# Kernel optimization log

Measured on AMD Instinct MI355X. Metric: run time of the kernel, lower is better.

Reference implementation:

```python
import jax, jax.numpy as jnp
import numpy as np

N_EMBED = 1024
HEAD_SIZE = 128

def setup_inputs() -> dict:
    key = jax.random.key(0)
    kx, kq, kk, kv = jax.random.split(key, 4)
    B, T = 8, 2048
    x = jax.random.normal(kx, (B, T, N_EMBED), dtype=jnp.float32)
    s = 1.0 / np.sqrt(N_EMBED)
    Wq = jax.random.normal(kq, (N_EMBED, HEAD_SIZE), dtype=jnp.float32) * s
    Wk = jax.random.normal(kk, (N_EMBED, HEAD_SIZE), dtype=jnp.float32) * s
    Wv = jax.random.normal(kv, (N_EMBED, HEAD_SIZE), dtype=jnp.float32) * s
    return {"x": x, "Wq": Wq, "Wk": Wk, "Wv": Wv}

def reference(x, Wq, Wk, Wv):
    # x: [B, T, E]; single-head causal attention (nanoGPT-style Head)
    B, T, E = x.shape
    q = jnp.einsum('bte,eh->bth', x, Wq)  # [B,T,H]
    k = jnp.einsum('bte,eh->bth', x, Wk)
    v = jnp.einsum('bte,eh->bth', x, Wv)
    scale = 1.0 / jnp.sqrt(jnp.asarray(q.shape[-1], dtype=x.dtype))
    wei = jnp.einsum('bqh,bkh->bqk', q, k) * scale  # [B,T,T]
    causal = jnp.tril(jnp.ones((T, T), dtype=bool))
    wei = jnp.where(causal[None, :, :], wei, jnp.asarray(-jnp.inf, dtype=wei.dtype))
    attn = jax.nn.softmax(wei, axis=-1)
    out = jnp.einsum('bqk,bkh->bqh', attn, v)  # [B,T,H]
    return out
```

## Files before the change

### kernel.cpp

```cpp
#include <hip/hip_runtime.h>
#include <hip/hip_bf16.h>

typedef __bf16 bf16_t;
typedef bf16_t bf16x8 __attribute__((ext_vector_type(8)));
typedef bf16_t bf16x4 __attribute__((ext_vector_type(4)));
typedef float f32x4 __attribute__((ext_vector_type(4)));

#define MFMA16(a, b, c) __builtin_amdgcn_mfma_f32_16x16x32_bf16((a), (b), (c), 0, 0, 0)

#define TT 2048
#define EE 1024
#define HH 128
#define UPB 576


__global__ __launch_bounds__(256) void prep_w_kernel(
    const float* __restrict__ Wq, const float* __restrict__ Wk,
    const float* __restrict__ Wv, bf16_t* __restrict__ Wf)
{
    int idx = blockIdx.x * 256 + threadIdx.x;
    int e  = idx & 7;
    int c  = (idx >> 3) & 15;
    int g  = (idx >> 7) & 3;
    int kt = (idx >> 9) & 31;
    int ct = idx >> 14;
    int w  = ct >> 3;
    const float* W = (w == 0) ? Wq : (w == 1) ? Wk : Wv;
    int k = kt * 32 + g * 8 + e;
    int n = (ct & 7) * 16 + c;
    Wf[idx] = (bf16_t)W[k * HH + n];
}

__global__ __launch_bounds__(256) void qkv_kernel(
    const float* __restrict__ x, const bf16_t* __restrict__ Wf,
    bf16_t* __restrict__ Qf, bf16_t* __restrict__ Kf, bf16_t* __restrict__ Vf)
{
    __shared__ __attribute__((aligned(16))) bf16_t As[2][64][72];
    const int bx = blockIdx.x;
    const int row0  = (bx & 255) * 64;
    const int nhalf = bx >> 8;
    const int tid  = threadIdx.x;
    const int lane = tid & 63;
    const int wn   = tid >> 6;
    const int g = lane >> 4, c = lane & 15;

    const int srow = tid >> 2;
    const int scg  = tid & 3;
    const float* xp = x + (size_t)(row0 + srow) * EE + scg * 16;

    const bf16_t* wfb = Wf + ((size_t)(nhalf * 12 + wn * 3) * 32) * 512 + lane * 8;

    f32x4 acc[4][3];
    for (int i = 0; i < 4; ++i)
        for (int j = 0; j < 3; ++j) acc[i][j] = (f32x4)0.0f;

    f32x4 xa[3][4];
    bf16x8 w[2][6];

#define BAR() do {                                                            \
    asm volatile("s_waitcnt lgkmcnt(0)" ::: "memory");                        \
    __builtin_amdgcn_s_barrier();                                             \
    __builtin_amdgcn_sched_barrier(0);                                        \
} while (0)
#define XLOAD(S, T)                                                           \
    for (int q = 0; q < 4; ++q)                                               \
        xa[S][q] = *(const f32x4*)(xp + (size_t)(T) * 64 + q * 4);
#define WLOAD(S, T)                                                           \
    for (int kk = 0; kk < 2; ++kk)                                            \
        for (int j = 0; j < 3; ++j)                                           \
            w[S][kk * 3 + j] = *(const bf16x8*)(wfb +                         \
                ((size_t)j * 32 + (T) * 2 + kk) * 512);
#define XWRITE(S, BUF) do {                                                   \
    union { bf16_t h[8]; unsigned long long u[2]; } pA_, pB_;                 \
    for (int q = 0; q < 4; ++q) {                                             \
        pA_.h[q]     = (bf16_t)xa[S][0][q];                                   \
        pA_.h[4 + q] = (bf16_t)xa[S][1][q];                                   \
        pB_.h[q]     = (bf16_t)xa[S][2][q];                                   \
        pB_.h[4 + q] = (bf16_t)xa[S][3][q];                                   \
    }                                                                         \
    *reinterpret_cast<unsigned long long*>(&As[BUF][srow][scg * 16])     = pA_.u[0]; \
    *reinterpret_cast<unsigned long long*>(&As[BUF][srow][scg * 16 + 4]) = pA_.u[1]; \
    *reinterpret_cast<unsigned long long*>(&As[BUF][srow][scg * 16 + 8]) = pB_.u[0]; \
    *reinterpret_cast<unsigned long long*>(&As[BUF][srow][scg * 16 +12]) = pB_.u[1]; \
} while (0)

    XLOAD(0, 0);
    XLOAD(1, 1);
    XLOAD(2, 2);
    WLOAD(0, 0);
    WLOAD(1, 1);
    XWRITE(0, 0);
    BAR();

#pragma unroll
    for (int t = 0; t < 16; ++t) {
        const int buf = t & 1;
        if (t + 3 < 16) XLOAD((t + 3) % 3, t + 3);
        __builtin_amdgcn_s_setprio(1);
        for (int kk = 0; kk < 2; ++kk)
            for (int mt = 0; mt < 4; ++mt) {
                bf16x8 af = *(const bf16x8*)&As[buf][mt * 16 + c][kk * 32 + g * 8];
                for (int j = 0; j < 3; ++j)
                    acc[mt][j] = MFMA16(af, w[t & 1][kk * 3 + j], acc[mt][j]);
            }
        __builtin_amdgcn_s_setprio(0);
        if (t + 2 < 16) WLOAD(t & 1, t + 2);
        if (t + 1 < 16) XWRITE((t + 1) % 3, buf ^ 1);
        BAR();
    }
#undef XLOAD
#undef WLOAD
#undef XWRITE
#undef BAR

    const float sc = 0.08838834764831845f * 1.4426950408889634f;
    for (int mt = 0; mt < 4; ++mt)
        for (int j = 0; j < 3; ++j) {
            int cb = nhalf * 192 + wn * 48 + j * 16;
            int w_ = cb >> 7;
            int hl = (cb & 127) + c;
            int t0 = row0 + mt * 16 + g * 4;
            if (w_ == 2) {
                int b  = t0 >> 11;
                int ttr = t0 & (TT - 1);
                int vc = ttr >> 5, gg = (ttr & 31) >> 3, j0 = ttr & 7;
                int hb = hl >> 4, cc = hl & 15;
                union { bf16_t h4[4]; unsigned long long u; } pk;
                for (int i = 0; i < 4; ++i) pk.h4[i] = (bf16_t)acc[mt][j][i];
                *reinterpret_cast<unsigned long long*>(
                    Vf + ((size_t)((b * 64 + vc) * 8 + hb)) * 512 +
                    (gg * 16 + cc) * 8 + j0) = pk.u;
            } else {
                bf16_t* dst = (w_ == 0) ? Qf : Kf;
                float s = (w_ == 0) ? sc : 1.0f;
                int kk = hl >> 5, gg = (hl & 31) >> 3, e = hl & 7;
                int grt = t0 >> 4;
                for (int i = 0; i < 4; ++i) {
                    int cr = (t0 + i) & 15;
                    dst[((size_t)(grt * 4 + kk)) * 512 + (gg * 16 + cr) * 8 + e] =
                        (bf16_t)(acc[mt][j][i] * s);
                }
            }
        }
}

__global__ __launch_bounds__(256) void attn_kernel(
    const bf16_t* __restrict__ Qf, const bf16_t* __restrict__ Kf,
    const bf16_t* __restrict__ Vf, bf16_t* __restrict__ Pacc,
    float* __restrict__ Pml)
{
    __shared__ __attribute__((aligned(16))) bf16_t Pl[4][16][40];
    const int tid = threadIdx.x, lane = tid & 63, wid = tid >> 6;
    const int g = lane >> 4, c = lane & 15;
    bf16_t (*P)[40] = Pl[wid];

    const int bx = blockIdx.x;
    const int b  = bx & 7;
    const int u  = 575 - ((bx >> 3) * 4 + wid);
    int k = 0;
    while (8 * (k + 1) * (k + 2) <= u) ++k;
    const int r  = u - 8 * k * (k + 1);
    const int qt = 16 * k + r / (k + 1);
    const int ch = r - (r / (k + 1)) * (k + 1);
    const int q0 = qt * 16;
    const int kv_lo = ch * 256;
    int kv_hi = kv_lo + 256; if (kv_hi > q0 + 16) kv_hi = q0 + 16;
    const int sid = b * UPB + 8 * k * (k + 1) + (qt & 15) * (k + 1) + ch;

    bf16x8 qf[4];
    for (int kk = 0; kk < 4; ++kk)
        qf[kk] = *(const bf16x8*)(Qf +
            ((size_t)((b * 128 + qt) * 4 + kk)) * 512 + lane * 8);

    f32x4 acc[8];
    for (int hb = 0; hb < 8; ++hb) acc[hb] = (f32x4)0.0f;
    float ls[4] = {0, 0, 0, 0};

    for (int kv0 = kv_lo; kv0 < kv_hi; kv0 += 32) {
        const int kt = b * 128 + (kv0 >> 4);
        bf16x8 k0f[4], k1f[4], vf[8];
        for (int kk = 0; kk < 4; ++kk) {
            k0f[kk] = *(const bf16x8*)(Kf + ((size_t)(kt * 4 + kk)) * 512 + lane * 8);
            k1f[kk] = *(const bf16x8*)(Kf + ((size_t)((kt + 1) * 4 + kk)) * 512 + lane * 8);
        }
        const int vcb = (b * 64 + (kv0 >> 5)) * 8;
        for (int hb = 0; hb < 8; ++hb)
            vf[hb] = *(const bf16x8*)(Vf + ((size_t)(vcb + hb)) * 512 + lane * 8);

        f32x4 s0 = (f32x4)0.0f, s1 = (f32x4)0.0f;
        for (int kk = 0; kk < 4; ++kk) {
            s0 = MFMA16(qf[kk], k0f[kk], s0);
            s1 = MFMA16(qf[kk], k1f[kk], s1);
        }
        if (kv0 + 32 > q0) {
            for (int i = 0; i < 4; ++i) {
                int row = q0 + g * 4 + i;
                if (kv0 + c > row)      s0[i] = -1e30f;
                if (kv0 + 16 + c > row) s1[i] = -1e30f;
            }
        }
        float p0[4], p1[4];
        for (int i = 0; i < 4; ++i) {
            p0[i] = exp2f(s0[i]);
            p1[i] = exp2f(s1[i]);
            ls[i] += p0[i] + p1[i];
        }
        for (int i = 0; i < 4; ++i) {
            P[g * 4 + i][c]      = (bf16_t)p0[i];
            P[g * 4 + i][c + 16] = (bf16_t)p1[i];
        }
        __builtin_amdgcn_wave_barrier();
        asm volatile("s_waitcnt lgkmcnt(0)" ::: "memory");
        __builtin_amdgcn_sched_barrier(0);
        bf16x8 pa = *(const bf16x8*)&P[c][g * 8];
        __builtin_amdgcn_s_setprio(1);
        for (int hb = 0; hb < 8; ++hb)
            acc[hb] = MFMA16(pa, vf[hb], acc[hb]);
        __builtin_amdgcn_s_setprio(0);
        __builtin_amdgcn_wave_barrier();
    }

    for (int off = 1; off < 16; off <<= 1)
        for (int i = 0; i < 4; ++i) ls[i] += __shfl_xor(ls[i], off, 64);
    if (c == 0)
        for (int i = 0; i < 4; ++i)
            Pml[(size_t)sid * 16 + g * 4 + i] = ls[i];

    bf16_t* po = Pacc + (size_t)sid * (16 * 128);
    for (int hb = 0; hb < 8; ++hb) {
        union { bf16_t h4[4]; unsigned long long u; } pk;
        for (int i = 0; i < 4; ++i) pk.h4[i] = (bf16_t)acc[hb][i];
        *reinterpret_cast<unsigned long long*>(
            po + (hb * 16 + c) * 16 + g * 4) = pk.u;
    }
}

__global__ __launch_bounds__(128) void combine_kernel(
    const bf16_t* __restrict__ Pacc, const float* __restrict__ Pml,
    float* __restrict__ out)
{
    __shared__ float invL[8];
    const int qt = blockIdx.x;
    const int b  = blockIdx.y;
    const int qz = blockIdx.z;
    const int k  = qt >> 4;
    const int base  = b * UPB + 8 * k * (k + 1) + (qt & 15) * (k + 1);
    const int count = k + 1;
    const int tid = threadIdx.x;

    if (tid < 8) {
        float L = 0.0f;
        for (int cu = 0; cu < count; ++cu)
            L += Pml[(size_t)(base + cu) * 16 + qz * 8 + tid];
        invL[tid] = 1.0f / L;
    }
    __syncthreads();

    float s[8];
    for (int r = 0; r < 8; ++r) s[r] = 0.0f;
    for (int cu = 0; cu < count; ++cu) {
        bf16x8 v = *(const bf16x8*)(
            Pacc + (size_t)(base + cu) * 2048 + tid * 16 + qz * 8);
        for (int j = 0; j < 8; ++j) s[j] += (float)v[j];
    }
    const int q0 = qt * 16 + qz * 8;
    for (int r = 0; r < 8; ++r)
        out[((size_t)b * TT + q0 + r) * HH + tid] = s[r] * invL[r];
}

extern "C" void kernel_launch(void* const* d_in, const int* in_sizes, int n_in,
                              void* d_out, int out_size, void* d_ws, size_t ws_size,
                              hipStream_t stream)
{
    const float* x  = (const float*)d_in[0];
    const float* Wq = (const float*)d_in[1];
    const float* Wk = (const float*)d_in[2];
    const float* Wv = (const float*)d_in[3];

    char* ws = (char*)d_ws;
    bf16_t* Wf   = (bf16_t*)ws;
    bf16_t* Qf   = (bf16_t*)(ws + (1u  << 20));
    bf16_t* Kf   = (bf16_t*)(ws + (5u  << 20));
    bf16_t* Vf   = (bf16_t*)(ws + (9u  << 20));
    bf16_t* Pacc = (bf16_t*)(ws + (13u << 20));
    float*  Pml  = (float*) (ws + (32u << 20));

    prep_w_kernel<<<1536, 256, 0, stream>>>(Wq, Wk, Wv, Wf);
    qkv_kernel<<<512, 256, 0, stream>>>(x, Wf, Qf, Kf, Vf);
    attn_kernel<<<1152, 256, 0, stream>>>(Qf, Kf, Vf, Pacc, Pml);
    combine_kernel<<<dim3(128, 8, 2), 128, 0, stream>>>(Pacc, Pml, (float*)d_out);
}
```

Before: 66.10 us.

## Stage x tiles via direct global-to-LDS loads with swizzle, convert at read

Replaces the register-staged x load (global to VGPR, convert to bf16, write to LDS) with global_load_lds DMA of fp32 tiles straight into an XOR-swizzled LDS buffer, double-buffered with vmcnt-based waits. Each wave then converts to bf16 when reading LDS fragments for the MFMAs. This is meant to free VGPRs and cut the VALU and LDS-write work in the staging path. In exchange it doubles LDS footprint and read bandwidth (fp32 instead of bf16), adds conversion work inside the MFMA loop, and prefetches only one tile ahead instead of three.

```diff
diff --git a/kernel.cpp b/kernel.cpp
--- a/kernel.cpp
+++ b/kernel.cpp
@@ -12,6 +12,9 @@
 #define EE 1024
 #define HH 128
 #define UPB 576
+
+typedef __attribute__((address_space(3))) void lds_void_t;
+typedef const __attribute__((address_space(1))) void gbl_void_t;
 
 
 __global__ __launch_bounds__(256) void prep_w_kernel(
@@ -35,88 +38,85 @@
     const float* __restrict__ x, const bf16_t* __restrict__ Wf,
     bf16_t* __restrict__ Qf, bf16_t* __restrict__ Kf, bf16_t* __restrict__ Vf)
 {
-    __shared__ __attribute__((aligned(16))) bf16_t As[2][64][72];
+    __shared__ __attribute__((aligned(16))) float As[2][64][64];
     const int bx = blockIdx.x;
     const int row0  = (bx & 255) * 64;
     const int nhalf = bx >> 8;
     const int tid  = threadIdx.x;
     const int lane = tid & 63;
-    const int wn   = tid >> 6;
+    const int wid  = tid >> 6;
     const int g = lane >> 4, c = lane & 15;
 
-    const int srow = tid >> 2;
-    const int scg  = tid & 3;
-    const float* xp = x + (size_t)(row0 + srow) * EE + scg * 16;
-
-    const bf16_t* wfb = Wf + ((size_t)(nhalf * 12 + wn * 3) * 32) * 512 + lane * 8;
+    const bf16_t* wfb = Wf + ((size_t)(nhalf * 12 + wid * 3) * 32) * 512 + lane * 8;
 
     f32x4 acc[4][3];
     for (int i = 0; i < 4; ++i)
         for (int j = 0; j < 3; ++j) acc[i][j] = (f32x4)0.0f;
 
-    f32x4 xa[3][4];
     bf16x8 w[2][6];
 
-#define BAR() do {                                                            \
-    asm volatile("s_waitcnt lgkmcnt(0)" ::: "memory");                        \
-    __builtin_amdgcn_s_barrier();                                             \
-    __builtin_amdgcn_sched_barrier(0);                                        \
-} while (0)
-#define XLOAD(S, T)                                                           \
-    for (int q = 0; q < 4; ++q)                                               \
-        xa[S][q] = *(const f32x4*)(xp + (size_t)(T) * 64 + q * 4);
+#define STAGE(BUF, T)                                                         \
+    for (int i = 0; i < 4; ++i) {                                             \
+        int srow = wid * 16 + i * 4 + (lane >> 4);                            \
+        int scol = (lane & 15) ^ (srow & 7);                                  \
+        __builtin_amdgcn_global_load_lds(                                     \
+            (gbl_void_t*)(x + (size_t)(row0 + srow) * EE + (size_t)(T) * 64 + scol * 4), \
+            (lds_void_t*)&As[BUF][wid * 16 + i * 4][0],                       \
+            16, 0, 0);                                                        \
+    }
 #define WLOAD(S, T)                                                           \
     for (int kk = 0; kk < 2; ++kk)                                            \
         for (int j = 0; j < 3; ++j)                                           \
             w[S][kk * 3 + j] = *(const bf16x8*)(wfb +                         \
                 ((size_t)j * 32 + (T) * 2 + kk) * 512);
-#define XWRITE(S, BUF) do {                                                   \
-    union { bf16_t h[8]; unsigned long long u[2]; } pA_, pB_;                 \
-    for (int q = 0; q < 4; ++q) {                                             \
-        pA_.h[q]     = (bf16_t)xa[S][0][q];                                   \
-        pA_.h[4 + q] = (bf16_t)xa[S][1][q];                                   \
-        pB_.h[q]     = (bf16_t)xa[S][2][q];                                   \
-        pB_.h[4 + q] = (bf16_t)xa[S][3][q];                                   \
-    }                                                                         \
-    *reinterpret_cast<unsigned long long*>(&As[BUF][srow][scg * 16])     = pA_.u[0]; \
-    *reinterpret_cast<unsigned long long*>(&As[BUF][srow][scg * 16 + 4]) = pA_.u[1]; \
-    *reinterpret_cast<unsigned long long*>(&As[BUF][srow][scg * 16 + 8]) = pB_.u[0]; \
-    *reinterpret_cast<unsigned long long*>(&As[BUF][srow][scg * 16 +12]) = pB_.u[1]; \
-} while (0)
-
-    XLOAD(0, 0);
-    XLOAD(1, 1);
-    XLOAD(2, 2);
+#define COMPUTE(BUF, S) do {                                                  \
+    for (int kk = 0; kk < 2; ++kk)                                            \
+        for (int mt = 0; mt < 4; ++mt) {                                      \
+            const char* rb = (const char*)&As[BUF][mt * 16 + c][0];           \
+            int s0 = kk * 8 + g * 2;                                          \
+            f32x4 r0 = *(const f32x4*)(rb + ((s0 ^ (c & 7)) << 4));           \
+            f32x4 r1 = *(const f32x4*)(rb + (((s0 + 1) ^ (c & 7)) << 4));     \
+            union { bf16_t h[8]; bf16x8 v; } u_;                              \
+            for (int q = 0; q < 4; ++q) {                                     \
+                u_.h[q]     = (bf16_t)r0[q];                                  \
+                u_.h[4 + q] = (bf16_t)r1[q];                                  \
+            }                                                                 \
+            for (int j = 0; j < 3; ++j)                                       \
+                acc[mt][j] = MFMA16(u_.v, w[S][kk * 3 + j], acc[mt][j]);      \
+        } } while (0)
+
     WLOAD(0, 0);
     WLOAD(1, 1);
-    XWRITE(0, 0);
-    BAR();
+    STAGE(0, 0);
+    asm volatile("s_waitcnt vmcnt(0)" ::: "memory");
+    __builtin_amdgcn_s_barrier();
+    __builtin_amdgcn_sched_barrier(0);
 
 #pragma unroll
     for (int t = 0; t < 16; ++t) {
         const int buf = t & 1;
-        if (t + 3 < 16) XLOAD((t + 3) % 3, t + 3);
+        if (t + 1 < 16) STAGE(buf ^ 1, t + 1);
+        if (t < 14)      asm volatile("s_waitcnt vmcnt(10)" ::: "memory");
+        else if (t < 15) asm volatile("s_waitcnt vmcnt(4)"  ::: "memory");
+        else             asm volatile("s_waitcnt vmcnt(0)"  ::: "memory");
+        __builtin_amdgcn_s_barrier();
+        __builtin_amdgcn_sched_barrier(0);
         __builtin_amdgcn_s_setprio(1);
-        for (int kk = 0; kk < 2; ++kk)
-            for (int mt = 0; mt < 4; ++mt) {
-                bf16x8 af = *(const bf16x8*)&As[buf][mt * 16 + c][kk * 32 + g * 8];
-                for (int j = 0; j < 3; ++j)
-                    acc[mt][j] = MFMA16(af, w[t & 1][kk * 3 + j], acc[mt][j]);
-            }
+        COMPUTE(buf, buf);
         __builtin_amdgcn_s_setprio(0);
-        if (t + 2 < 16) WLOAD(t & 1, t + 2);
-        if (t + 1 < 16) XWRITE((t + 1) % 3, buf ^ 1);
-        BAR();
-    }
-#undef XLOAD
+        if (t + 2 < 16) WLOAD(buf, t + 2);
+        asm volatile("s_waitcnt lgkmcnt(0)" ::: "memory");
+        __builtin_amdgcn_s_barrier();
+        __builtin_amdgcn_sched_barrier(0);
+    }
+#undef STAGE
 #undef WLOAD
-#undef XWRITE
-#undef BAR
+#undef COMPUTE
 
     const float sc = 0.08838834764831845f * 1.4426950408889634f;
     for (int mt = 0; mt < 4; ++mt)
         for (int j = 0; j < 3; ++j) {
-            int cb = nhalf * 192 + wn * 48 + j * 16;
+            int cb = nhalf * 192 + wid * 48 + j * 16;
             int w_ = cb >> 7;
             int hl = (cb & 127) + c;
             int t0 = row0 + mt * 16 + g * 4;
```

New measurement: 65.09 us. Within noise of the previous version (-1.5%).
